# Kernel optimization log

Measured on AMD Instinct MI355X. Metric: run time of the kernel, lower is better.

Reference implementation:

```python
import jax, jax.numpy as jnp
import numpy as np
from jax import lax

RADIUS = 0.3
NSAMPLE = 16
NPROP = 256
NHB = 12
NSC = 18
NCLS = 18
BNEPS = 1e-5


def setup_inputs() -> dict:
    key = jax.random.key(0)
    ks = jax.random.split(key, 10)
    B, K, C = 32, 2048, 256
    OUT = 2 + 3 + NHB * 2 + NSC * 4 + NCLS  # 119
    return {
        "xyz": jax.random.uniform(ks[0], (B, K, 3), jnp.float32),
        "features": jax.random.normal(ks[1], (B, C, K), jnp.float32),
        "sa_w1": jax.random.normal(ks[2], (256, C + 3), jnp.float32) * 0.05,
        "sa_w2": jax.random.normal(ks[3], (256, 256), jnp.float32) * 0.05,
        "sa_w3": jax.random.normal(ks[4], (256, 256), jnp.float32) * 0.05,
        "sa_gamma": jnp.ones((3, 256), jnp.float32),
        "sa_beta": jnp.zeros((3, 256), jnp.float32),
        "sa_mean": jnp.zeros((3, 256), jnp.float32),
        "sa_var": jnp.ones((3, 256), jnp.float32),
        "p_w1": jax.random.normal(ks[5], (256, 256), jnp.float32) * 0.05,
        "p_w2": jax.random.normal(ks[6], (256, 256), jnp.float32) * 0.05,
        "p_w3": jax.random.normal(ks[7], (OUT, 256), jnp.float32) * 0.05,
        "p_b3": jnp.zeros((OUT,), jnp.float32),
        "p_gamma": jnp.ones((2, 256), jnp.float32),
        "p_beta": jnp.zeros((2, 256), jnp.float32),
        "p_mean": jnp.zeros((2, 256), jnp.float32),
        "p_var": jnp.ones((2, 256), jnp.float32),
        "mean_size_arr": jax.random.uniform(ks[8], (NSC, 3), jnp.float32, 0.3, 1.5),
    }


def fps(xyz, npoint):
    # iterative furthest point sampling, starts at index 0 (matches CUDA kernel)
    B, K, _ = xyz.shape

    def body(carry, _):
        dist, far = carry
        centroid = jnp.take_along_axis(xyz, far[:, None, None], axis=1)  # (B,1,3)
        d = jnp.sum((xyz - centroid) ** 2, axis=-1)  # (B,K)
        dist = jnp.minimum(dist, d)
        nxt = jnp.argmax(dist, axis=-1).astype(jnp.int32)
        return (dist, nxt), far

    init = (jnp.full((B, K), 1e10, xyz.dtype), jnp.zeros((B,), jnp.int32))
    _, inds = lax.scan(body, init, None, length=npoint)
    return jnp.transpose(inds, (1, 0))  # (B, npoint)


def ball_query(new_xyz, xyz):
    # first NSAMPLE points (in original index order) within RADIUS; pad with first hit
    B, K, _ = xyz.shape
    d2 = jnp.sum((new_xyz[:, :, None, :] - xyz[:, None, :, :]) ** 2, axis=-1)  # (B,P,K)
    within = d2 < RADIUS * RADIUS
    cand = jnp.where(within, jnp.arange(K, dtype=jnp.int32)[None, None, :], K)
    cand = jnp.sort(cand, axis=-1)[..., :NSAMPLE]
    first = cand[..., :1]  # query point itself is always within radius
    return jnp.where(cand == K, first, cand)  # (B,P,NSAMPLE)


def box_corners(center_unnorm, size, angle):
    # flip_axis_to_camera: X right, Y down (-z_up), Z forward (y_up)
    cc = jnp.stack([center_unnorm[..., 0], center_unnorm[..., 2], -center_unnorm[..., 1]], axis=-1)
    c, s = jnp.cos(angle), jnp.sin(angle)
    zz, oo = jnp.zeros_like(angle), jnp.ones_like(angle)
    R = jnp.stack([c, zz, s, zz, oo, zz, -s, zz, c], axis=-1).reshape(angle.shape + (3, 3))
    sx = jnp.asarray([1, 1, -1, -1, 1, 1, -1, -1], jnp.float32)
    sy = jnp.asarray([1, 1, 1, 1, -1, -1, -1, -1], jnp.float32)
    sz = jnp.asarray([1, -1, -1, 1, 1, -1, -1, 1], jnp.float32)
    xc = size[..., 0:1] * sx * 0.5
    yc = size[..., 2:3] * sy * 0.5
    zc = size[..., 1:2] * sz * 0.5
    corners = jnp.stack([xc, yc, zc], axis=-2)  # (B,P,3,8)
    out = jnp.einsum('bpij,bpjk->bpik', R, corners) + cc[..., None]
    return jnp.transpose(out, (0, 1, 3, 2))  # (B,P,8,3)


def _forward(xyz, features, sa_w1, sa_w2, sa_w3, sa_gamma, sa_beta, sa_mean, sa_var,
             p_w1, p_w2, p_w3, p_b3, p_gamma, p_beta, p_mean, p_var, mean_size_arr):
    B, K, _ = xyz.shape
    inds = fps(xyz, NPROP)  # (B,P) vote_fps
    new_xyz = jnp.take_along_axis(xyz, inds[..., None], axis=1)  # (B,P,3)
    idx = ball_query(new_xyz, xyz)  # (B,P,S)
    flat = idx.reshape(B, -1)
    g_xyz = jnp.take_along_axis(xyz, flat[..., None], axis=1).reshape(B, NPROP, NSAMPLE, 3)
    g_xyz = (g_xyz - new_xyz[:, :, None, :]) / RADIUS  # normalize_xyz
    g_feat = jnp.take_along_axis(features, flat[:, None, :], axis=2).reshape(B, -1, NPROP, NSAMPLE)
    x = jnp.concatenate([jnp.transpose(g_xyz, (0, 3, 1, 2)), g_feat], axis=1)  # (B,3+C,P,S)
    for i, w in enumerate((sa_w1, sa_w2, sa_w3)):
        x = jnp.einsum('oc,bcps->bops', w, x)
        scale = (sa_gamma[i] / jnp.sqrt(sa_var[i] + BNEPS))[None, :, None, None]
        x = jax.nn.relu((x - sa_mean[i][None, :, None, None]) * scale + sa_beta[i][None, :, None, None])
    y = jnp.max(x, axis=-1)  # (B,256,P) max-pool over neighbors
    for i, w in enumerate((p_w1, p_w2)):
        y = jnp.einsum('oc,bcp->bop', w, y)
        scale = (p_gamma[i] / jnp.sqrt(p_var[i] + BNEPS))[None, :, None]
        y = jax.nn.relu((y - p_mean[i][None, :, None]) * scale + p_beta[i][None, :, None])
    net = jnp.einsum('oc,bcp->bop', p_w3, y) + p_b3[None, :, None]
    nt = jnp.transpose(net, (0, 2, 1))  # (B,P,119)
    obj = nt[..., 0:2]
    center = new_xyz + nt[..., 2:5]
    o = 5 + NHB * 2
    size_scores = nt[..., o:o + NSC]
    srn = nt[..., o + NSC:o + NSC * 4].reshape(B, NPROP, NSC, 3)
    sem = nt[..., o + NSC * 4:]
    size_res = srn * mean_size_arr[None, None]
    best = jnp.argmax(size_scores, axis=-1)
    pred_size = jnp.take_along_axis(size_res + mean_size_arr[None, None],
                                    best[..., None, None], axis=2)[:, :, 0, :]
    corners = box_corners(center, pred_size, jnp.zeros_like(center[..., 0]))
    sem_logits = jnp.concatenate(
        [sem, jnp.argmin(obj, axis=-1, keepdims=True).astype(nt.dtype) * 1e10], axis=-1)
    obj_prob = jax.nn.softmax(obj, axis=-1)[..., 1]
    sem_prob = jax.nn.softmax(sem, axis=-1)
    return obj, center, size_scores, size_res, pred_size, sem, corners, sem_logits, obj_prob, sem_prob


def reference(xyz, features, sa_w1, sa_w2, sa_w3, sa_gamma, sa_beta, sa_mean, sa_var,
              p_w1, p_w2, p_w3, p_b3, p_gamma, p_beta, p_mean, p_var, mean_size_arr):
    return _forward(xyz, features, sa_w1, sa_w2, sa_w3, sa_gamma, sa_beta, sa_mean, sa_var,
                    p_w1, p_w2, p_w3, p_b3, p_gamma, p_beta, p_mean, p_var, mean_size_arr)
```

## Files before the change

kernel.cpp:

```cpp
#include <hip/hip_runtime.h>
#include <math.h>

#define B_   32
#define K_   2048
#define C_   256
#define P_   256
#define S_   16
#define OUTC 119

#define OFF0 0
#define OFF1 16384
#define OFF2 40960
#define OFF3 188416
#define OFF4 630784
#define OFF5 655360
#define OFF6 802816
#define OFF7 999424
#define OFF8 1155072
#define OFF9 1163264

typedef _Float16 half8  __attribute__((ext_vector_type(8)));
typedef _Float16 half4h __attribute__((ext_vector_type(4)));
typedef float    f32x4  __attribute__((ext_vector_type(4)));
typedef float    f32x2  __attribute__((ext_vector_type(2)));
#define MFMA16 __builtin_amdgcn_mfma_f32_16x16x32_f16

#define XT 65

__device__ __forceinline__ float sqdist_rn(float ax, float ay, float az,
                                           float bx, float by, float bz) {
  float dx = __fsub_rn(ax, bx), dy = __fsub_rn(ay, by), dz = __fsub_rn(az, bz);
  return __fadd_rn(__fadd_rn(__fmul_rn(dx, dx), __fmul_rn(dy, dy)),
                   __fmul_rn(dz, dz));
}

__device__ __forceinline__ unsigned umax_(unsigned a, unsigned b) {
  return a > b ? a : b;
}
__device__ __forceinline__ unsigned umin_(unsigned a, unsigned b) {
  return a < b ? a : b;
}

__device__ __forceinline__ void wsplit_body(
    int r, int t, const float* __restrict__ w1, const float* __restrict__ w2,
    const float* __restrict__ w3, const float* __restrict__ pw1,
    const float* __restrict__ pw2, const float* __restrict__ gma,
    const float* __restrict__ var, const float* __restrict__ pg,
    const float* __restrict__ pv, _Float16* __restrict__ w1h,
    _Float16* __restrict__ w1l, _Float16* __restrict__ w2h,
    _Float16* __restrict__ w2l, _Float16* __restrict__ w3h,
    _Float16* __restrict__ w3l, _Float16* __restrict__ p1h,
    _Float16* __restrict__ p1l, _Float16* __restrict__ p2h,
    _Float16* __restrict__ p2l, float* __restrict__ bns) {
  if (r == 656) {
    for (int u = t; u < 768; u += 64) bns[u] = gma[u] / sqrtf(var[u] + 1e-5f);
    for (int u = t; u < 512; u += 64)
      bns[768 + u] = pg[u] / sqrtf(pv[u] + 1e-5f);
    return;
  }
  const float* src;
  _Float16 *dh, *dl;
  int ot, ks, nks, K, remap = 0;
  if (r < 144) {
    src = w1; dh = w1h; dl = w1l; ot = r / 9; ks = r % 9; nks = 9; K = 259;
    remap = 1;
  } else if (r < 272) {
    const int rr = r - 144;
    src = w2; dh = w2h; dl = w2l; ot = rr >> 3; ks = rr & 7; nks = 8; K = 256;
  } else if (r < 400) {
    const int rr = r - 272;
    src = w3; dh = w3h; dl = w3l; ot = rr >> 3; ks = rr & 7; nks = 8; K = 256;
  } else if (r < 528) {
    const int rr = r - 400;
    src = pw1; dh = p1h; dl = p1l; ot = rr >> 3; ks = rr & 7; nks = 8; K = 256;
  } else {
    const int rr = r - 528;
    src = pw2; dh = p2h; dl = p2l; ot = rr >> 3; ks = rr & 7; nks = 8; K = 256;
  }
  const int m = t & 15, q = t >> 4;
  const float* row = src + (ot * 16 + m) * K;
  half8 vh, vl;
#pragma unroll
  for (int j = 0; j < 8; j++) {
    const int c = ks * 32 + q * 8 + j;
    float v;
    if (remap) {
      v = (c < 3) ? row[c] : (c >= 8 && c < 264) ? row[c - 5] : 0.f;
    } else {
      v = (c < K) ? row[c] : 0.f;
    }
    const _Float16 hi = (_Float16)v;
    vh[j] = hi;
    vl[j] = (_Float16)(v - (float)hi);
  }
  const int base = ((ot * nks + ks) * 64 + t) * 8;
  *(half8*)&dh[base] = vh;
  *(half8*)&dl[base] = vl;
}

__global__ __launch_bounds__(256) void fused_pre_kernel(
    const float* __restrict__ xyz, float* __restrict__ new_xyz,
    const float* __restrict__ features, _Float16* __restrict__ ftH,
    _Float16* __restrict__ ftL,
    const float* __restrict__ w1, const float* __restrict__ w2,
    const float* __restrict__ w3, const float* __restrict__ pw1,
    const float* __restrict__ pw2, const float* __restrict__ gma,
    const float* __restrict__ var, const float* __restrict__ pg,
    const float* __restrict__ pv, _Float16* __restrict__ w1h,
    _Float16* __restrict__ w1l, _Float16* __restrict__ w2h,
    _Float16* __restrict__ w2l, _Float16* __restrict__ w3h,
    _Float16* __restrict__ w3l, _Float16* __restrict__ p1h,
    _Float16* __restrict__ p1l, _Float16* __restrict__ p2h,
    _Float16* __restrict__ p2l, float* __restrict__ bns) {
  __shared__ __align__(16) char smem_pre[32768];
  __shared__ __align__(16) unsigned long long redk[2][4];
  const int bid = blockIdx.x;

  if (bid >= 197) {
    const int idx = bid - 197;
    const int b = idx >> 7, rem = idx & 127;
    const int c0 = (rem >> 5) * 64, k0 = (rem & 31) * 64;
    float* tl = (float*)smem_pre;
    const int w = threadIdx.x >> 6, lane = threadIdx.x & 63;
    const float* fb = features + (size_t)b * C_ * K_;
#pragma unroll
    for (int r = 0; r < 16; r++) {
      const int cl = r * 4 + w;
      tl[cl * 65 + lane] = fb[(size_t)(c0 + cl) * K_ + k0 + lane];
    }
    __syncthreads();
#pragma unroll
    for (int r = 0; r < 16; r++) {
      const int kl = r * 4 + w;
      const float v = tl[lane * 65 + kl];
      const _Float16 hi = (_Float16)v;
      const size_t o = ((size_t)b * K_ + k0 + kl) * C_ + c0 + lane;
      ftH[o] = hi;
      ftL[o] = (_Float16)(v - (float)hi);
    }
    return;
  }

  if (bid >= 32) {
    const int sub = (bid - 32) * 4 + (threadIdx.x >> 6);
    if (sub < 657)
      wsplit_body(sub, threadIdx.x & 63, w1, w2, w3, pw1, pw2, gma, var, pg,
                  pv, w1h, w1l, w2h, w2l, w3h, w3l, p1h, p1l, p2h, p2l, bns);
    return;
  }

  const int b = bid, t = threadIdx.x;
  const int lane = t & 63, w = t >> 6;
  float4* pts = (float4*)smem_pre;
  const float* xb = xyz + b * K_ * 3;
  f32x2 px[4], py[4], pz[4], dist[4];
#pragma unroll
  for (int j = 0; j < 8; j++) {
    const int k = t + 256 * j;
    const float x = xb[3 * k + 0];
    const float yv = xb[3 * k + 1];
    const float z = xb[3 * k + 2];
    px[j >> 1][j & 1] = x;
    py[j >> 1][j & 1] = yv;
    pz[j >> 1][j & 1] = z;
    dist[j >> 1][j & 1] = 1e10f;
    pts[k] = make_float4(x, yv, z, 0.f);
  }
  __syncthreads();
  int far = 0;
  for (int i = 0; i < P_; i++) {
    const float4 c = pts[far];
    if (t == 0) {
      float* nx = new_xyz + (b * P_ + i) * 3;
      nx[0] = c.x; nx[1] = c.y; nx[2] = c.z;
    }
    {
#pragma clang fp contract(off)
      const f32x2 cx = {c.x, c.x}, cy = {c.y, c.y}, cz = {c.z, c.z};
#pragma unroll
      for (int j2 = 0; j2 < 4; j2++) {
        const f32x2 dx = px[j2] - cx;
        const f32x2 dy = py[j2] - cy;
        const f32x2 dz = pz[j2] - cz;
        const f32x2 d = (dx * dx + dy * dy) + dz * dz;
        dist[j2] = __builtin_elementwise_min(dist[j2], d);
      }
    }
    unsigned long long bkey = 0ull;
#pragma unroll
    for (int j2 = 0; j2 < 4; j2++)
#pragma unroll
      for (int e = 0; e < 2; e++) {
        const unsigned kg = (unsigned)((2 * j2 + e) * 256 + t);
        const unsigned long long key =
            ((unsigned long long)__float_as_uint(dist[j2][e]) << 32) |
            (unsigned long long)(0xFFFFFFFFu - kg);
        bkey = (key > bkey) ? key : bkey;
      }
#define RSTEP(ctl)                                                            \
  {                                                                           \
    const unsigned olo = (unsigned)__builtin_amdgcn_update_dpp(               \
        0, (int)(unsigned)bkey, ctl, 0xf, 0xf, false);                        \
    const unsigned ohi = (unsigned)__builtin_amdgcn_update_dpp(               \
        0, (int)(unsigned)(bkey >> 32), ctl, 0xf, 0xf, false);                \
    const unsigned long long o = ((unsigned long long)ohi << 32) | olo;       \
    bkey = (o > bkey) ? o : bkey;                                             \
  }
    RSTEP(0x111) RSTEP(0x112) RSTEP(0x114) RSTEP(0x118)
    RSTEP(0x142) RSTEP(0x143)
#undef RSTEP
    if (lane == 63) redk[i & 1][w] = bkey;
    __syncthreads();
    const unsigned long long k0 = redk[i & 1][0], k1 = redk[i & 1][1];
    const unsigned long long k2 = redk[i & 1][2], k3 = redk[i & 1][3];
    unsigned long long km = (k0 > k1) ? k0 : k1;
    km = (k2 > km) ? k2 : km;
    km = (k3 > km) ? k3 : km;
    far = (int)(0xFFFFFFFFu - (unsigned)(km & 0xFFFFFFFFull));
  }
}

__global__ __launch_bounds__(1024) void ballq_kernel(
    const float* __restrict__ xyz, const float* __restrict__ new_xyz,
    int* __restrict__ idxw) {
  const int blk = blockIdx.x;
  const int b = blk >> 4, pg = (blk & 15) * 16, t = threadIdx.x;
  __shared__ __align__(16) float4 pts[K_];
  const float* xb = xyz + b * K_ * 3;
#pragma unroll
  for (int j = 0; j < 2; j++) {
    const int k = t + 1024 * j;
    pts[k] = make_float4(xb[3 * k + 0], xb[3 * k + 1], xb[3 * k + 2], 0.f);
  }
  __syncthreads();
  const float r2 = (float)(0.3 * 0.3);
  const int w = t >> 6, lane = t & 63;
  const int p = pg + w;
  const float nx = new_xyz[(b * P_ + p) * 3 + 0];
  const float ny = new_xyz[(b * P_ + p) * 3 + 1];
  const float nz = new_xyz[(b * P_ + p) * 3 + 2];
  int* ob = idxw + (b * P_ + p) * S_;
  unsigned msk = 0u;
#pragma unroll
  for (int j = 0; j < 32; j++) {
    const float4 q = pts[j * 64 + lane];
    const float d2 = sqdist_rn(q.x, q.y, q.z, nx, ny, nz);
    msk |= (d2 < r2 ? 1u : 0u) << j;
  }
  int cnt = 0, first = -1;
  for (int j = 0; j < 32; j++) {
    const unsigned long long bal = __ballot((msk >> j) & 1u);
    if (bal != 0ull && first < 0) first = j * 64 + (__ffsll(bal) - 1);
    const int c = (int)__popcll(bal);
    if ((msk >> j) & 1u) {
      const int pos = cnt + (int)__popcll(bal & ((1ull << lane) - 1ull));
      if (pos < S_) ob[pos] = j * 64 + lane;
    }
    cnt += c;
    if (cnt >= S_) break;
  }
  if (cnt < S_ && lane < S_ - cnt) ob[cnt + lane] = first;
}

__global__ __launch_bounds__(512, 4) void sa_kernel(
    const float* __restrict__ xyz, const float* __restrict__ features,
    const _Float16* __restrict__ ftH, const _Float16* __restrict__ ftL,
    const int use_ft,
    const _Float16* __restrict__ w1h, const _Float16* __restrict__ w1l,
    const _Float16* __restrict__ w2h, const _Float16* __restrict__ w2l,
    const _Float16* __restrict__ w3h, const _Float16* __restrict__ w3l,
    const float* __restrict__ bns, const float* __restrict__ mu,
    const float* __restrict__ bta, const float* __restrict__ new_xyz,
    const int* __restrict__ idxw, float* __restrict__ y) {
  const int blk = blockIdx.x;
  const int b = blk >> 6, p0 = (blk & 63) * 4, t = threadIdx.x;
  __shared__ __align__(16) _Float16 Xh[36 * XT * 8];
  __shared__ __align__(16) _Float16 Xl[36 * XT * 8];
  __shared__ __align__(16) float red[4 * 256];
  __shared__ int k_sh[64];

  if (t < 64) k_sh[t] = idxw[(b * P_ + p0) * S_ + t];
  if (t < 192) {
    const int tile = 32 + t / 48, row = 16 + (t % 48);
    const half8 z8 = {};
    *(half8*)&Xh[(tile * XT + row) * 8] = z8;
    *(half8*)&Xl[(tile * XT + row) * 8] = z8;
  }
  __syncthreads();
  if (t < 64) {
    const int st = t >> 4, m = t & 15, k = k_sh[t];
    const float* xb = xyz + b * K_ * 3;
    const float* nx = new_xyz + (b * P_ + p0 + st) * 3;
    const int base = (st * XT + m) * 8;
#pragma unroll
    for (int c = 0; c < 3; c++) {
      const float v = (xb[3 * k + c] - nx[c]) / 0.3f;
      const _Float16 hi = (_Float16)v;
      Xh[base + c] = hi;
      Xl[base + c] = (_Float16)(v - (float)hi);
    }
#pragma unroll
    for (int j = 3; j < 8; j++) {
      Xh[base + j] = (_Float16)0.f;
      Xl[base + j] = (_Float16)0.f;
    }
  }
  if (use_ft) {
    for (int u = t; u < 2048; u += 512) {
      const int s = u >> 5, ch = u & 31;
      const int c = 8 + ch * 8;
      const int ks = c >> 5, q2 = (c >> 3) & 3;
      const int st = s >> 4, m = s & 15;
      const size_t ro = ((size_t)b * K_ + k_sh[s]) * C_ + ch * 8;
      const int row = (q2 * 16 + m) ^ (ks & 7);
      const int dst = ((ks * 4 + st) * XT + row) * 8;
      *(half8*)&Xh[dst] = *(const half8*)&ftH[ro];
      *(half8*)&Xl[dst] = *(const half8*)&ftL[ro];
    }
  } else {
    const int cl = t & 255, hf = t >> 8;
    const float* fb = features + (size_t)b * C_ * K_ + (size_t)cl * K_;
    const int c = 8 + cl;
    const int ks = c >> 5, q2 = (c >> 3) & 3, j = c & 7;
    const int s0 = hf * 32;
#pragma unroll 8
    for (int s = s0; s < s0 + 32; s++) {
      const float v = fb[k_sh[s]];
      const _Float16 hi = (_Float16)v;
      const int row = (q2 * 16 + (s & 15)) ^ (ks & 7);
      const int dst = ((ks * 4 + (s >> 4)) * XT + row) * 8 + j;
      Xh[dst] = hi;
      Xl[dst] = (_Float16)(v - (float)hi);
    }
  }

  const int lane = t & 63, w = t >> 6;
  const int m = lane & 15, q = lane >> 4;
  const int og = w & 3, sg = w >> 2;

  f32x4 acc[4][2];
  half8 rAh[2][4], rAl[2][4];
#pragma unroll
  for (int i = 0; i < 4; i++) {
    const int off = (((og * 4 + i) * 9 + 0) * 64 + lane) * 8;
    rAh[0][i] = *(const half8*)&w1h[off];
    rAl[0][i] = *(const half8*)&w1l[off];
  }
  __syncthreads();

#pragma unroll
  for (int l = 0; l < 3; l++) {
    const int nks = (l == 0) ? 9 : 8;
    const int base = (l == 0) ? 0 : (l == 1) ? 9 : 17;
#pragma unroll
    for (int i = 0; i < 4; i++) {
      acc[i][0] = (f32x4){0.f, 0.f, 0.f, 0.f};
      acc[i][1] = (f32x4){0.f, 0.f, 0.f, 0.f};
    }
#pragma unroll
    for (int ks = 0; ks < nks; ks++) {
      const int par = (base + ks) & 1;
      {
        int ln = l, kn = ks + 1;
        if (kn >= nks) { kn = 0; ln = l + 1; }
        if (ln < 3) {
          const _Float16* Ph = (ln == 0) ? w1h : (ln == 1) ? w2h : w3h;
          const _Float16* Pl = (ln == 0) ? w1l : (ln == 1) ? w2l : w3l;
          const int nk2 = (ln == 0) ? 9 : 8;
#pragma unroll
          for (int i = 0; i < 4; i++) {
            const int off = (((og * 4 + i) * nk2 + kn) * 64 + lane) * 8;
            rAh[par ^ 1][i] = *(const half8*)&Ph[off];
            rAl[par ^ 1][i] = *(const half8*)&Pl[off];
          }
        }
      }
      const int rsw = lane ^ (ks & 7);
#pragma unroll
      for (int s = 0; s < 2; s++) {
        const int tb = ((ks * 4 + sg * 2 + s) * XT + rsw) * 8;
        const half8 Bh = *(const half8*)&Xh[tb];
        const half8 Bl = *(const half8*)&Xl[tb];
#pragma unroll
        for (int i = 0; i < 4; i++) {
          acc[i][s] = MFMA16(rAh[par][i], Bh, acc[i][s], 0, 0, 0);
          acc[i][s] = MFMA16(rAh[par][i], Bl, acc[i][s], 0, 0, 0);
          acc[i][s] = MFMA16(rAl[par][i], Bh, acc[i][s], 0, 0, 0);
        }
      }
    }

    if (l < 2) {
      __syncthreads();
#pragma unroll
      for (int i = 0; i < 4; i++) {
        const int c0 = (og * 4 + i) * 16 + q * 4;
        const int ks2 = c0 >> 5, q2 = (c0 >> 3) & 3, j0 = c0 & 7;
        const f32x4 sc4 = *(const f32x4*)&bns[l * 256 + c0];
        const f32x4 m4 = *(const f32x4*)&mu[l * 256 + c0];
        const f32x4 b4 = *(const f32x4*)&bta[l * 256 + c0];
        const int row = (q2 * 16 + m) ^ (ks2 & 7);
#pragma unroll
        for (int s = 0; s < 2; s++) {
          half4h vh, vl;
#pragma unroll
          for (int r = 0; r < 4; r++) {
            const float v = fmaxf((acc[i][s][r] - m4[r]) * sc4[r] + b4[r], 0.f);
            const _Float16 hi = (_Float16)v;
            vh[r] = hi;
            vl[r] = (_Float16)(v - (float)hi);
          }
          const int dst = ((ks2 * 4 + sg * 2 + s) * XT + row) * 8 + j0;
          *(half4h*)&Xh[dst] = vh;
          *(half4h*)&Xl[dst] = vl;
        }
      }
      __syncthreads();
    } else {
#pragma unroll
      for (int i = 0; i < 4; i++)
#pragma unroll
        for (int s = 0; s < 2; s++)
#pragma unroll
          for (int r = 0; r < 4; r++) {
            float v = acc[i][s][r];
            v = fmaxf(v, __shfl_xor(v, 1));
            v = fmaxf(v, __shfl_xor(v, 2));
            v = fmaxf(v, __shfl_xor(v, 4));
            v = fmaxf(v, __shfl_xor(v, 8));
            acc[i][s][r] = v;
          }
      if (m == 0) {
#pragma unroll
        for (int i = 0; i < 4; i++) {
          const int ob = (og * 4 + i) * 16 + q * 4;
#pragma unroll
          for (int s = 0; s < 2; s++)
            *(f32x4*)&red[(sg * 2 + s) * 256 + ob] = acc[i][s];
        }
      }
      __syncthreads();
      for (int u = t; u < 1024; u += 512) {
        const int pl = u >> 8, col = u & 255;
        const float sc2 = bns[512 + col];
        const float mu2 = mu[512 + col], bt2 = bta[512 + col];
        const float raw = red[pl * 256 + col];
        y[(b * P_ + p0 + pl) * 256 + col] = fmaxf((raw - mu2) * sc2 + bt2, 0.f);
      }
    }
  }
}

__global__ __launch_bounds__(256, 2) void phead_kernel(
    const float* __restrict__ y, const _Float16* __restrict__ p1h,
    const _Float16* __restrict__ p1l, const _Float16* __restrict__ p2h,
    const _Float16* __restrict__ p2l, const float* __restrict__ pw3,
    const float* __restrict__ pb3, const float* __restrict__ bns,
    const float* __restrict__ pm, const float* __restrict__ pb,
    const float* __restrict__ new_xyz, const float* __restrict__ msa,
    float* __restrict__ out) {
  const int blk = blockIdx.x;
  const int b = blk >> 4, p0 = (blk & 15) * 16, t = threadIdx.x;
  __shared__ __align__(16) char smem[58624];
  _Float16* X0h = (_Float16*)smem;
  _Float16* X0l = (_Float16*)(smem + 8448);
  _Float16* Hh  = (_Float16*)(smem + 16896);
  _Float16* Hl  = (_Float16*)(smem + 25344);
  float*    Wt  = (float*)smem;
  float*    Y2  = (float*)(smem + 33792);
  float*    net_s = (float*)(smem + 50432);

  {
#pragma unroll 4
    for (int s = 0; s < 16; s++) {
      const float v = y[(size_t)(b * P_ + p0 + s) * C_ + t];
      const _Float16 hi = (_Float16)v;
      X0h[s * 264 + t] = hi;
      X0l[s * 264 + t] = (_Float16)(v - (float)hi);
    }
  }
  const int lane = t & 63, w = t >> 6;
  const int m = lane & 15, q = lane >> 4;

  f32x4 acc[4];
  half8 pAh[4], pAl[4];
#pragma unroll
  for (int i = 0; i < 4; i++) {
    const int off = (((4 * w + i) * 8) * 64 + lane) * 8;
    pAh[i] = *(const half8*)&p1h[off];
    pAl[i] = *(const half8*)&p1l[off];
  }
  __syncthreads();

#pragma unroll
  for (int l = 0; l < 2; l++) {
    const _Float16* Xih = l ? Hh : X0h;
    const _Float16* Xil = l ? Hl : X0l;
#pragma unroll
    for (int i = 0; i < 4; i++) acc[i] = (f32x4){0.f, 0.f, 0.f, 0.f};
    for (int ks = 0; ks < 8; ks++) {
      half8 Ah[4], Al[4];
#pragma unroll
      for (int i = 0; i < 4; i++) { Ah[i] = pAh[i]; Al[i] = pAl[i]; }
      {
        int ln = l, kn = ks + 1;
        if (kn == 8) { ln = l + 1; kn = 0; }
        if (ln < 2) {
          const _Float16* Ph = ln ? p2h : p1h;
          const _Float16* Pl = ln ? p2l : p1l;
#pragma unroll
          for (int i = 0; i < 4; i++) {
            const int off = (((4 * w + i) * 8 + kn) * 64 + lane) * 8;
            pAh[i] = *(const half8*)&Ph[off];
            pAl[i] = *(const half8*)&Pl[off];
          }
        }
      }
      const int xo = ks * 32 + q * 8;
      const half8 Bh = *(const half8*)&Xih[m * 264 + xo];
      const half8 Bl = *(const half8*)&Xil[m * 264 + xo];
#pragma unroll
      for (int i = 0; i < 4; i++) {
        acc[i] = MFMA16(Ah[i], Bh, acc[i], 0, 0, 0);
        acc[i] = MFMA16(Ah[i], Bl, acc[i], 0, 0, 0);
        acc[i] = MFMA16(Al[i], Bh, acc[i], 0, 0, 0);
      }
    }
#pragma unroll
    for (int i = 0; i < 4; i++) {
      const int ob = (4 * w + i) * 16 + q * 4;
      const f32x4 sc4 = *(const f32x4*)&bns[768 + l * 256 + ob];
      const f32x4 m4 = *(const f32x4*)&pm[l * 256 + ob];
      const f32x4 b4 = *(const f32x4*)&pb[l * 256 + ob];
      if (l == 0) {
        half4h vh, vl;
#pragma unroll
        for (int r = 0; r < 4; r++) {
          const float v = fmaxf((acc[i][r] - m4[r]) * sc4[r] + b4[r], 0.f);
          const _Float16 hi = (_Float16)v;
          vh[r] = hi;
          vl[r] = (_Float16)(v - (float)hi);
        }
        *(half4h*)&Hh[m * 264 + ob] = vh;
        *(half4h*)&Hl[m * 264 + ob] = vl;
      } else {
        f32x4 r4;
#pragma unroll
        for (int r = 0; r < 4; r++)
          r4[r] = fmaxf((acc[i][r] - m4[r]) * sc4[r] + b4[r], 0.f);
        *(f32x4*)&Y2[m * 260 + ob] = r4;
      }
    }
    __syncthreads();
  }

  {
    const int o = t & 127, ph = t >> 7;
    float a3[8];
#pragma unroll
    for (int pp = 0; pp < 8; pp++) a3[pp] = 0.f;
    for (int tile = 0; tile < 16; tile++) {
      const int c0 = tile * 16;
      for (int u = t; u < 119 * 4; u += 256) {
        int oo = u >> 2, qq = u & 3;
        *(float4*)&Wt[(qq * 128 + oo) * 4] =
            *(const float4*)(pw3 + oo * 256 + c0 + qq * 4);
      }
      __syncthreads();
      if (o < 119) {
#pragma unroll
        for (int j4 = 0; j4 < 4; j4++) {
          const float4 wv = *(const float4*)&Wt[(j4 * 128 + o) * 4];
#pragma unroll
          for (int pp = 0; pp < 8; pp++) {
            const float4 xv =
                *(const float4*)&Y2[(ph * 8 + pp) * 260 + c0 + j4 * 4];
            a3[pp] = fmaf(wv.x, xv.x, a3[pp]);
            a3[pp] = fmaf(wv.y, xv.y, a3[pp]);
            a3[pp] = fmaf(wv.z, xv.z, a3[pp]);
            a3[pp] = fmaf(wv.w, xv.w, a3[pp]);
          }
        }
      }
      __syncthreads();
    }
    if (o < 119) {
      const float bb = pb3[o];
#pragma unroll
      for (int pp = 0; pp < 8; pp++)
        net_s[(ph * 8 + pp) * 120 + o] = a3[pp] + bb;
    }
  }
  __syncthreads();

  if (t < 16) {
    const int gi = b * P_ + p0 + t;
    const float* nr = &net_s[t * 120];
    const float nx = new_xyz[gi * 3 + 0];
    const float ny = new_xyz[gi * 3 + 1];
    const float nz = new_xyz[gi * 3 + 2];
    const float obj0 = nr[0], obj1 = nr[1];
    out[OFF0 + gi * 2 + 0] = obj0;
    out[OFF0 + gi * 2 + 1] = obj1;
    const float cx = nx + nr[2], cy = ny + nr[3], cz = nz + nr[4];
    out[OFF1 + gi * 3 + 0] = cx;
    out[OFF1 + gi * 3 + 1] = cy;
    out[OFF1 + gi * 3 + 2] = cz;
    float bv = -1e30f;
    int bi = 0;
#pragma unroll
    for (int i = 0; i < 18; i++) {
      float v = nr[29 + i];
      out[OFF2 + gi * 18 + i] = v;
      if (v > bv) { bv = v; bi = i; }
    }
#pragma unroll
    for (int i = 0; i < 18; i++)
#pragma unroll
      for (int j = 0; j < 3; j++)
        out[OFF3 + gi * 54 + i * 3 + j] =
            __fmul_rn(nr[47 + i * 3 + j], msa[i * 3 + j]);
    float ps[3];
#pragma unroll
    for (int j = 0; j < 3; j++) {
      ps[j] = __fadd_rn(__fmul_rn(nr[47 + bi * 3 + j], msa[bi * 3 + j]),
                        msa[bi * 3 + j]);
      out[OFF4 + gi * 3 + j] = ps[j];
    }
    float sm = -1e30f;
#pragma unroll
    for (int i = 0; i < 18; i++) {
      float v = nr[101 + i];
      out[OFF5 + gi * 18 + i] = v;
      out[OFF7 + gi * 19 + i] = v;
      sm = fmaxf(sm, v);
    }
    out[OFF7 + gi * 19 + 18] = (obj0 <= obj1) ? 0.f : 1e10f;
    const float cc0 = cx, cc1 = cz, cc2 = -cy;
    const float sxk[8] = {1, 1, -1, -1, 1, 1, -1, -1};
    const float syk[8] = {1, 1, 1, 1, -1, -1, -1, -1};
    const float szk[8] = {1, -1, -1, 1, 1, -1, -1, 1};
#pragma unroll
    for (int k = 0; k < 8; k++) {
      out[OFF6 + gi * 24 + 3 * k + 0] = cc0 + ps[0] * sxk[k] * 0.5f;
      out[OFF6 + gi * 24 + 3 * k + 1] = cc1 + ps[2] * syk[k] * 0.5f;
      out[OFF6 + gi * 24 + 3 * k + 2] = cc2 + ps[1] * szk[k] * 0.5f;
    }
    {
      const float m2 = fmaxf(obj0, obj1);
      const float e0 = expf(obj0 - m2), e1 = expf(obj1 - m2);
      out[OFF8 + gi] = e1 / (e0 + e1);
    }
    {
      float ev[18], es = 0.f;
#pragma unroll
      for (int i = 0; i < 18; i++) {
        ev[i] = expf(nr[101 + i] - sm);
        es += ev[i];
      }
#pragma unroll
      for (int i = 0; i < 18; i++) out[OFF9 + gi * 18 + i] = ev[i] / es;
    }
  }
}

extern "C" void kernel_launch(void* const* d_in, const int* in_sizes, int n_in,
                              void* d_out, int out_size, void* d_ws,
                              size_t ws_size, hipStream_t stream) {
  (void)in_sizes; (void)n_in; (void)out_size;
  const float* xyz      = (const float*)d_in[0];
  const float* features = (const float*)d_in[1];
  const float* w1       = (const float*)d_in[2];
  const float* w2       = (const float*)d_in[3];
  const float* w3       = (const float*)d_in[4];
  const float* gma      = (const float*)d_in[5];
  const float* bta      = (const float*)d_in[6];
  const float* mu       = (const float*)d_in[7];
  const float* var      = (const float*)d_in[8];
  const float* pw1      = (const float*)d_in[9];
  const float* pw2      = (const float*)d_in[10];
  const float* pw3      = (const float*)d_in[11];
  const float* pb3      = (const float*)d_in[12];
  const float* pg       = (const float*)d_in[13];
  const float* pb       = (const float*)d_in[14];
  const float* pm       = (const float*)d_in[15];
  const float* pv       = (const float*)d_in[16];
  const float* msa      = (const float*)d_in[17];
  float* out = (float*)d_out;

  char* ws = (char*)d_ws;
  float*     new_xyz = (float*)ws;
  int*       idxw    = (int*)(ws + 98304);
  float*     yb      = (float*)(ws + 622592);
  _Float16*  w1h     = (_Float16*)(ws + 9011200);
  _Float16*  w1l     = (_Float16*)(ws + 9158656);
  _Float16*  w2h     = (_Float16*)(ws + 9306112);
  _Float16*  w2l     = (_Float16*)(ws + 9437184);
  _Float16*  w3h     = (_Float16*)(ws + 9568256);
  _Float16*  w3l     = (_Float16*)(ws + 9699328);
  float*     bns     = (float*)(ws + 9830400);
  _Float16*  p1h     = (_Float16*)(ws + 9835520);
  _Float16*  p1l     = (_Float16*)(ws + 9966592);
  _Float16*  p2h     = (_Float16*)(ws + 10097664);
  _Float16*  p2l     = (_Float16*)(ws + 10228736);
  _Float16*  ftH     = (_Float16*)(ws + 10359808);
  _Float16*  ftL     = (_Float16*)(ws + 43914240);

  const int use_ft = (ws_size >= 77468672ull) ? 1 : 0;
  const int npre = use_ft ? (197 + 4096) : 197;

  fused_pre_kernel<<<npre, 256, 0, stream>>>(xyz, new_xyz, features, ftH, ftL,
                                             w1, w2, w3, pw1, pw2, gma, var,
                                             pg, pv, w1h, w1l, w2h, w2l, w3h,
                                             w3l, p1h, p1l, p2h, p2l, bns);
  ballq_kernel<<<B_ * 16, 1024, 0, stream>>>(xyz, new_xyz, idxw);
  sa_kernel<<<B_ * 64, 512, 0, stream>>>(xyz, features, ftH, ftL, use_ft,
                                         w1h, w1l, w2h, w2l, w3h, w3l, bns,
                                         mu, bta, new_xyz, idxw, yb);
  phead_kernel<<<B_ * 16, 256, 0, stream>>>(yb, p1h, p1l, p2h, p2l, pw3, pb3,
                                            bns, pm, pb, new_xyz, msa, out);
}
```

Measured before the change: 455.5 us.

## Repartition SA MLP warps to two output tiles and prefetch weights two steps ahead

```diff
diff --git a/kernel.cpp b/kernel.cpp
--- a/kernel.cpp
+++ b/kernel.cpp
@@ -336,15 +336,15 @@
 
   const int lane = t & 63, w = t >> 6;
   const int m = lane & 15, q = lane >> 4;
-  const int og = w & 3, sg = w >> 2;
-
-  f32x4 acc[4][2];
-  half8 rAh[2][4], rAl[2][4];
-#pragma unroll
-  for (int i = 0; i < 4; i++) {
-    const int off = (((og * 4 + i) * 9 + 0) * 64 + lane) * 8;
-    rAh[0][i] = *(const half8*)&w1h[off];
-    rAl[0][i] = *(const half8*)&w1l[off];
+
+  f32x4 acc[2][4];
+  half8 rAh[2][2], rAl[2][2];
+#pragma unroll
+  for (int i = 0; i < 2; i++) {
+    rAh[0][i] = *(const half8*)&w1h[(((2 * w + i) * 9 + 0) * 64 + lane) * 8];
+    rAl[0][i] = *(const half8*)&w1l[(((2 * w + i) * 9 + 0) * 64 + lane) * 8];
+    rAh[1][i] = *(const half8*)&w1h[(((2 * w + i) * 9 + 1) * 64 + lane) * 8];
+    rAl[1][i] = *(const half8*)&w1l[(((2 * w + i) * 9 + 1) * 64 + lane) * 8];
   }
   __syncthreads();
 
@@ -353,39 +353,41 @@
     const int nks = (l == 0) ? 9 : 8;
     const int base = (l == 0) ? 0 : (l == 1) ? 9 : 17;
 #pragma unroll
-    for (int i = 0; i < 4; i++) {
-      acc[i][0] = (f32x4){0.f, 0.f, 0.f, 0.f};
-      acc[i][1] = (f32x4){0.f, 0.f, 0.f, 0.f};
-    }
+    for (int i = 0; i < 2; i++)
+#pragma unroll
+      for (int s = 0; s < 4; s++) acc[i][s] = (f32x4){0.f, 0.f, 0.f, 0.f};
 #pragma unroll
     for (int ks = 0; ks < nks; ks++) {
       const int par = (base + ks) & 1;
+      half8 Ah[2], Al[2];
+#pragma unroll
+      for (int i = 0; i < 2; i++) { Ah[i] = rAh[par][i]; Al[i] = rAl[par][i]; }
       {
-        int ln = l, kn = ks + 1;
-        if (kn >= nks) { kn = 0; ln = l + 1; }
+        int ln = l, kn = ks + 2;
+        if (kn >= nks) { kn -= nks; ln = l + 1; }
         if (ln < 3) {
           const _Float16* Ph = (ln == 0) ? w1h : (ln == 1) ? w2h : w3h;
           const _Float16* Pl = (ln == 0) ? w1l : (ln == 1) ? w2l : w3l;
           const int nk2 = (ln == 0) ? 9 : 8;
 #pragma unroll
-          for (int i = 0; i < 4; i++) {
-            const int off = (((og * 4 + i) * nk2 + kn) * 64 + lane) * 8;
-            rAh[par ^ 1][i] = *(const half8*)&Ph[off];
-            rAl[par ^ 1][i] = *(const half8*)&Pl[off];
+          for (int i = 0; i < 2; i++) {
+            const int off = (((2 * w + i) * nk2 + kn) * 64 + lane) * 8;
+            rAh[par][i] = *(const half8*)&Ph[off];
+            rAl[par][i] = *(const half8*)&Pl[off];
           }
         }
       }
       const int rsw = lane ^ (ks & 7);
 #pragma unroll
-      for (int s = 0; s < 2; s++) {
-        const int tb = ((ks * 4 + sg * 2 + s) * XT + rsw) * 8;
+      for (int s = 0; s < 4; s++) {
+        const int tb = ((ks * 4 + s) * XT + rsw) * 8;
         const half8 Bh = *(const half8*)&Xh[tb];
         const half8 Bl = *(const half8*)&Xl[tb];
 #pragma unroll
-        for (int i = 0; i < 4; i++) {
-          acc[i][s] = MFMA16(rAh[par][i], Bh, acc[i][s], 0, 0, 0);
-          acc[i][s] = MFMA16(rAh[par][i], Bl, acc[i][s], 0, 0, 0);
-          acc[i][s] = MFMA16(rAl[par][i], Bh, acc[i][s], 0, 0, 0);
+        for (int i = 0; i < 2; i++) {
+          acc[i][s] = MFMA16(Ah[i], Bh, acc[i][s], 0, 0, 0);
+          acc[i][s] = MFMA16(Ah[i], Bl, acc[i][s], 0, 0, 0);
+          acc[i][s] = MFMA16(Al[i], Bh, acc[i][s], 0, 0, 0);
         }
       }
     }
@@ -393,15 +395,15 @@
     if (l < 2) {
       __syncthreads();
 #pragma unroll
-      for (int i = 0; i < 4; i++) {
-        const int c0 = (og * 4 + i) * 16 + q * 4;
+      for (int i = 0; i < 2; i++) {
+        const int c0 = (2 * w + i) * 16 + q * 4;
         const int ks2 = c0 >> 5, q2 = (c0 >> 3) & 3, j0 = c0 & 7;
         const f32x4 sc4 = *(const f32x4*)&bns[l * 256 + c0];
         const f32x4 m4 = *(const f32x4*)&mu[l * 256 + c0];
         const f32x4 b4 = *(const f32x4*)&bta[l * 256 + c0];
         const int row = (q2 * 16 + m) ^ (ks2 & 7);
 #pragma unroll
-        for (int s = 0; s < 2; s++) {
+        for (int s = 0; s < 4; s++) {
           half4h vh, vl;
 #pragma unroll
           for (int r = 0; r < 4; r++) {
@@ -410,7 +412,7 @@
             vh[r] = hi;
             vl[r] = (_Float16)(v - (float)hi);
           }
-          const int dst = ((ks2 * 4 + sg * 2 + s) * XT + row) * 8 + j0;
+          const int dst = ((ks2 * 4 + s) * XT + row) * 8 + j0;
           *(half4h*)&Xh[dst] = vh;
           *(half4h*)&Xl[dst] = vl;
         }
@@ -418,9 +420,9 @@
       __syncthreads();
     } else {
 #pragma unroll
-      for (int i = 0; i < 4; i++)
-#pragma unroll
-        for (int s = 0; s < 2; s++)
+      for (int i = 0; i < 2; i++)
+#pragma unroll
+        for (int s = 0; s < 4; s++)
 #pragma unroll
           for (int r = 0; r < 4; r++) {
             float v = acc[i][s][r];
@@ -432,11 +434,10 @@
           }
       if (m == 0) {
 #pragma unroll
-        for (int i = 0; i < 4; i++) {
-          const int ob = (og * 4 + i) * 16 + q * 4;
-#pragma unroll
-          for (int s = 0; s < 2; s++)
-            *(f32x4*)&red[(sg * 2 + s) * 256 + ob] = acc[i][s];
+        for (int i = 0; i < 2; i++) {
+          const int ob = (2 * w + i) * 16 + q * 4;
+#pragma unroll
+          for (int s = 0; s < 4; s++) *(f32x4*)&red[s * 256 + ob] = acc[i][s];
         }
       }
       __syncthreads();
```

New measurement: 433.6 us. 1.05x faster.
